# Performance work log

Hardware: AMD Instinct MI355X
Metric: run time of the kernel (lower is better)

## Reference

```python
import jax, jax.numpy as jnp
import numpy as np

N_EXPERTS = 8
TOP_K = 2


def setup_inputs() -> dict:
    key = jax.random.key(0)
    k1, k2, k3, k4 = jax.random.split(key, 4)
    B, T, C, H, E = 2, 2048, 1024, 4096, N_EXPERTS
    x = jax.random.normal(k1, (B, T, C), dtype=jnp.float32)
    # weights scaled like standard init to keep activations well-behaved
    router_w = jax.random.normal(k2, (E, C), dtype=jnp.float32) * 0.02
    w1 = jax.random.normal(k3, (E, C, H), dtype=jnp.float32) * (1.0 / np.sqrt(C))
    w2 = jax.random.normal(k4, (E, H, C), dtype=jnp.float32) * (1.0 / np.sqrt(H))
    return {"x": x, "router_w": router_w, "w1": w1, "w2": w2}


def reference(x, router_w, w1, w2):
    B, T, C = x.shape
    E = N_EXPERTS
    xf = x.reshape(-1, C)                                   # [N, C], N = B*T
    logits = jnp.einsum('nc,ec->ne', xf, router_w)          # router (no bias)
    probs = jax.nn.softmax(logits, axis=-1)
    top_w, top_i = jax.lax.top_k(probs, TOP_K)              # [N, K]
    top_w = top_w / jnp.sum(top_w, axis=-1, keepdims=True)  # renormalize
    # combine weight per (token, expert): sum of top-k weights routed to e
    comb = jnp.einsum('nk,nke->ne', top_w, jax.nn.one_hot(top_i, E, dtype=xf.dtype))
    # dense all-expert compute (bias=False, exact GELU, dropout=0 at eval)
    h = jax.nn.gelu(jnp.einsum('nc,ech->enh', xf, w1), approximate=False)  # [E, N, H]
    y = jnp.einsum('enh,ehc->enc', h, w2)                   # [E, N, C]
    out = jnp.einsum('ne,enc->nc', comb, y)                 # weighted combine
    return out.reshape(B, T, C)
```

## Files before the change

### kernel.cpp

```cpp
#include <hip/hip_runtime.h>
#include <hip/hip_bf16.h>
#include <stdint.h>

#define NTOK 4096
#define CD   1024
#define HD   4096
#define NE   8

typedef __attribute__((ext_vector_type(8))) short bf16x8;
typedef __attribute__((ext_vector_type(4))) float f32x4;
typedef __attribute__((ext_vector_type(4))) unsigned short us4;

__device__ __forceinline__ unsigned short f2bf(float f){
  __hip_bfloat16 h = __float2bfloat16(f);
  return *reinterpret_cast<unsigned short*>(&h);
}

__global__ __launch_bounds__(256) void router_kernel(
    const float* __restrict__ x, const float* __restrict__ rw,
    unsigned short* __restrict__ x_bf, int* __restrict__ top_i,
    float* __restrict__ top_w, int* __restrict__ counts){
  __shared__ float rw_lds[NE*CD];
  int tid = threadIdx.x;
  for (int i = tid; i < NE*CD/4; i += 256)
    ((float4*)rw_lds)[i] = ((const float4*)rw)[i];
  __syncthreads();
  int l = tid & 63, w = tid >> 6;
  int n = blockIdx.x*4 + w;

  float4 xv[4];
  #pragma unroll
  for (int j = 0; j < 4; ++j)
    xv[j] = ((const float4*)(x + (size_t)n*CD))[l + j*64];

  #pragma unroll
  for (int j = 0; j < 4; ++j){
    us4 o; o.x = f2bf(xv[j].x); o.y = f2bf(xv[j].y); o.z = f2bf(xv[j].z); o.w = f2bf(xv[j].w);
    *(us4*)(x_bf + (size_t)n*CD + l*4 + j*256) = o;
  }

  double le[NE];
  #pragma unroll
  for (int e = 0; e < NE; ++e){
    double p = 0.0;
    #pragma unroll
    for (int j = 0; j < 4; ++j){
      float4 rv = ((const float4*)(rw_lds + e*CD))[l + j*64];
      p += (double)xv[j].x*rv.x + (double)xv[j].y*rv.y + (double)xv[j].z*rv.z + (double)xv[j].w*rv.w;
    }
    #pragma unroll
    for (int d = 32; d >= 1; d >>= 1) p += __shfl_xor(p, d);
    le[e] = p;
  }
  if (l == 0){
    double m = le[0];
    #pragma unroll
    for (int e = 1; e < NE; ++e) m = le[e] > m ? le[e] : m;
    double pe[NE];
    #pragma unroll
    for (int e = 0; e < NE; ++e) pe[e] = exp(le[e]-m);
    int i0 = 0;
    #pragma unroll
    for (int e = 1; e < NE; ++e) if (pe[e] > pe[i0]) i0 = e;
    int i1 = (i0 == 0) ? 1 : 0;
    #pragma unroll
    for (int e = 0; e < NE; ++e){ if (e == i0) continue; if (pe[e] > pe[i1]) i1 = e; }
    double w0 = pe[i0], w1v = pe[i1], wsum = w0 + w1v;
    top_i[2*n] = i0; top_i[2*n+1] = i1;
    top_w[2*n] = (float)(w0/wsum); top_w[2*n+1] = (float)(w1v/wsum);
    atomicAdd(&counts[i0], 1); atomicAdd(&counts[i1], 1);
  }
}

__global__ void scan_kernel(const int* __restrict__ counts, int* __restrict__ offsets, int* __restrict__ cursor){
  if (threadIdx.x == 0){
    int s = 0;
    for (int e = 0; e < NE; ++e){ offsets[e] = s; cursor[e] = s; s += counts[e]; }
  }
}

__global__ __launch_bounds__(256) void scatter_kernel(
    const int* __restrict__ top_i, const float* __restrict__ top_w,
    int* __restrict__ cursor, int* __restrict__ g_tok, float* __restrict__ g_w){
  int n = blockIdx.x*256 + threadIdx.x;
  #pragma unroll
  for (int k = 0; k < 2; ++k){
    int e = top_i[2*n+k];
    int pos = atomicAdd(&cursor[e], 1);
    g_tok[pos] = n;
    g_w[pos] = top_w[2*n+k];
  }
}

template<int R, int S>
__global__ __launch_bounds__(256) void transpose_cvt(const float* __restrict__ in, unsigned short* __restrict__ outp){
  __shared__ float tile[64][65];
  int e = blockIdx.z;
  const float* ip = in + (size_t)e*R*S;
  unsigned short* op = outp + (size_t)e*R*S;
  int s0 = blockIdx.x*64, r0 = blockIdx.y*64;
  int tid = threadIdx.x;
  #pragma unroll
  for (int i = 0; i < 4; ++i){
    int lin = i*256 + tid;
    int rr = lin >> 4, c4 = lin & 15;
    float4 v = *(const float4*)(ip + (size_t)(r0+rr)*S + s0 + c4*4);
    tile[rr][c4*4+0] = v.x; tile[rr][c4*4+1] = v.y;
    tile[rr][c4*4+2] = v.z; tile[rr][c4*4+3] = v.w;
  }
  __syncthreads();
  #pragma unroll
  for (int i = 0; i < 4; ++i){
    int lin = i*256 + tid;
    int ss = lin >> 4, rq = lin & 15;
    us4 o;
    o.x = f2bf(tile[rq*4+0][ss]);
    o.y = f2bf(tile[rq*4+1][ss]);
    o.z = f2bf(tile[rq*4+2][ss]);
    o.w = f2bf(tile[rq*4+3][ss]);
    *(us4*)(op + (size_t)(s0+ss)*R + r0 + rq*4) = o;
  }
}

template<int KLEN, int SPLITK, int EPI>
__global__ __launch_bounds__(512, 6) void gemm2ph(
    const unsigned short* __restrict__ A_src,
    const unsigned short* __restrict__ B_src,
    unsigned short* __restrict__ h_out,
    float* __restrict__ outp,
    const int* __restrict__ g_tok,
    const float* __restrict__ g_w,
    const int* __restrict__ counts,
    const int* __restrict__ offsets,
    int NDIM, int KSTRIDE){
  constexpr int NT = KLEN/32;
  __shared__ alignas(128) char lds[32768];

  int z = blockIdx.z;
  int e  = (SPLITK == 1) ? z : (z / SPLITK);
  int kz = (SPLITK == 1) ? 0 : (z % SPLITK);
  int n_e = counts[e];
  int m0 = blockIdx.y*128;
  if (m0 >= n_e) return;
  int n0 = blockIdx.x*128;
  int g_base = offsets[e];
  int kstart = kz*KLEN;

  int tid = threadIdx.x, l = tid & 63, w = tid >> 6;
  int wr = w >> 2, wc = w & 3;
  int lrow = l & 15, q = l >> 4;

  const unsigned short* src[2];
  uint32_t dst[2];
  #pragma unroll
  for (int i = 0; i < 2; ++i){
    int g = i*512 + tid;
    bool isA = g < 512;
    int gg = isA ? g : (g - 512);
    int row = gg >> 2, c = gg & 3;
    int cs = c ^ (row & 3);
    if (isA){
      int rg = m0 + row; if (rg > n_e-1) rg = n_e-1;
      size_t arow;
      if (EPI == 0) arow = (size_t)g_tok[g_base + rg];
      else          arow = (size_t)(g_base + rg);
      src[i] = A_src + arow*(size_t)KSTRIDE + kstart + cs*8;
    } else {
      src[i] = B_src + ((size_t)e*NDIM + n0 + row)*(size_t)KSTRIDE + kstart + cs*8;
    }
    dst[i] = (uint32_t)g*16u;
  }

  uint32_t a_off[4], b_off[2];
  #pragma unroll
  for (int m = 0; m < 4; ++m){
    int ra = wr*64 + m*16 + lrow;
    a_off[m] = (uint32_t)(ra*64) + 16u*(q ^ (ra & 3));
  }
  #pragma unroll
  for (int n = 0; n < 2; ++n){
    int rb = wc*32 + n*16 + lrow;
    b_off[n] = 8192u + (uint32_t)(rb*64) + 16u*(q ^ (rb & 3));
  }

  f32x4 acc[4][2] = {};

  #pragma unroll
  for (int i = 0; i < 2; ++i){
    __builtin_amdgcn_global_load_lds((const __attribute__((address_space(1))) void*)src[i],
                                     (__attribute__((address_space(3))) void*)&lds[dst[i]], 16, 0, 0);
    src[i] += 32;
  }
  __syncthreads();

  uint32_t buf = 0;
  #pragma unroll 1
  for (int kt = 0; kt < NT; ++kt){
    if (kt + 1 < NT){
      uint32_t nb = (buf ^ 1)*16384u;
      #pragma unroll
      for (int i = 0; i < 2; ++i){
        __builtin_amdgcn_global_load_lds((const __attribute__((address_space(1))) void*)src[i],
                                         (__attribute__((address_space(3))) void*)&lds[dst[i] + nb], 16, 0, 0);
        src[i] += 32;
      }
    }
    uint32_t ro = buf*16384u;
    bf16x8 av[4], bv[2];
    #pragma unroll
    for (int m = 0; m < 4; ++m)
      av[m] = *(const bf16x8*)&lds[a_off[m] + ro];
    #pragma unroll
    for (int n = 0; n < 2; ++n)
      bv[n] = *(const bf16x8*)&lds[b_off[n] + ro];
    __builtin_amdgcn_s_setprio(1);
    #pragma unroll
    for (int m = 0; m < 4; ++m)
      #pragma unroll
      for (int n = 0; n < 2; ++n)
        acc[m][n] = __builtin_amdgcn_mfma_f32_16x16x32_bf16(av[m], bv[n], acc[m][n], 0, 0, 0);
    __builtin_amdgcn_s_setprio(0);
    __syncthreads();
    buf ^= 1;
  }

  if (EPI == 0){
    #pragma unroll
    for (int m = 0; m < 4; ++m){
      #pragma unroll
      for (int j = 0; j < 4; ++j){
        int r = m0 + wr*64 + m*16 + q*4 + j;
        if (r < n_e){
          unsigned short* hp = h_out + (size_t)(g_base + r)*NDIM + n0 + wc*32 + lrow;
          #pragma unroll
          for (int n = 0; n < 2; ++n){
            float v = acc[m][n][j];
            v = 0.5f*v*(1.0f + erff(v*0.70710678118654752f));
            hp[n*16] = f2bf(v);
          }
        }
      }
    }
  } else {
    #pragma unroll
    for (int m = 0; m < 4; ++m){
      #pragma unroll
      for (int j = 0; j < 4; ++j){
        int r = m0 + wr*64 + m*16 + q*4 + j;
        if (r < n_e){
          int slot = g_base + r;
          int t = g_tok[slot];
          float wgt = g_w[slot];
          float* op = outp + (size_t)t*NDIM + n0 + wc*32 + lrow;
          #pragma unroll
          for (int n = 0; n < 2; ++n)
            atomicAdd(op + n*16, wgt*acc[m][n][j]);
        }
      }
    }
  }
}

extern "C" void kernel_launch(void* const* d_in, const int* in_sizes, int n_in,
                              void* d_out, int out_size, void* d_ws, size_t ws_size,
                              hipStream_t stream) {
  const float* x  = (const float*)d_in[0];
  const float* rw = (const float*)d_in[1];
  const float* w1 = (const float*)d_in[2];
  const float* w2 = (const float*)d_in[3];

  size_t off = 0;
  auto alloc = [&](size_t sz) -> char* {
    char* p = (char*)d_ws + off;
    off += (sz + 255) & ~(size_t)255;
    return p;
  };
  unsigned short* x_bf = (unsigned short*)alloc((size_t)NTOK*CD*2);
  unsigned short* w1t  = (unsigned short*)alloc((size_t)NE*CD*HD*2);
  unsigned short* w2t  = (unsigned short*)alloc((size_t)NE*CD*HD*2);
  unsigned short* hbuf = (unsigned short*)alloc((size_t)NTOK*2*HD*2);
  int*   top_i  = (int*)alloc(NTOK*2*4);
  float* top_w  = (float*)alloc(NTOK*2*4);
  int*   counts = (int*)alloc(64);
  int*   offs   = (int*)alloc(64);
  int*   cursor = (int*)alloc(64);
  int*   g_tok  = (int*)alloc(NTOK*2*4);
  float* g_w    = (float*)alloc(NTOK*2*4);
  (void)ws_size; (void)in_sizes; (void)n_in; (void)out_size;

  hipMemsetAsync(d_out, 0, (size_t)NTOK*CD*4, stream);
  hipMemsetAsync(counts, 0, 64, stream);

  router_kernel<<<dim3(NTOK/4), dim3(256), 0, stream>>>(x, rw, x_bf, top_i, top_w, counts);
  scan_kernel<<<dim3(1), dim3(64), 0, stream>>>(counts, offs, cursor);
  scatter_kernel<<<dim3(NTOK/256), dim3(256), 0, stream>>>(top_i, top_w, cursor, g_tok, g_w);

  transpose_cvt<CD, HD><<<dim3(HD/64, CD/64, NE), dim3(256), 0, stream>>>(w1, w1t);
  transpose_cvt<HD, CD><<<dim3(CD/64, HD/64, NE), dim3(256), 0, stream>>>(w2, w2t);

  gemm2ph<CD, 1, 0><<<dim3(HD/128, 12, NE), dim3(512), 0, stream>>>(
      x_bf, w1t, hbuf, (float*)nullptr, g_tok, g_w, counts, offs, HD, CD);
  gemm2ph<HD/2, 2, 1><<<dim3(CD/128, 12, NE*2), dim3(512), 0, stream>>>(
      hbuf, w2t, (unsigned short*)nullptr, (float*)d_out, g_tok, g_w, counts, offs, CD, HD);
}
```

Before: 477.9 us.

## Use three-stage LDS ring with explicit vmcnt waits in grouped GEMMs

Replaces the double-buffered LDS pipeline with a three-slot ring buffer that prefetches two k-tiles ahead. It waits with explicit s_waitcnt vmcnt counts and issues a single raw s_barrier per iteration, where the old loop had a full __syncthreads at the end. The goal is to keep more global-to-LDS loads in flight and cut barrier stalls. In exchange LDS per block grows from 32KB to 48KB, which may lower occupancy. The hand-written waitcnt values assume the compiler emits exactly two loads per stage.

```diff
diff --git a/kernel.cpp b/kernel.cpp
--- a/kernel.cpp
+++ b/kernel.cpp
@@ -10,6 +10,10 @@
 typedef __attribute__((ext_vector_type(8))) short bf16x8;
 typedef __attribute__((ext_vector_type(4))) float f32x4;
 typedef __attribute__((ext_vector_type(4))) unsigned short us4;
+
+#define BARR() asm volatile("s_barrier" ::: "memory")
+#define VM2() asm volatile("s_waitcnt vmcnt(2)" ::: "memory")
+#define VM0() asm volatile("s_waitcnt vmcnt(0)" ::: "memory")
 
 __device__ __forceinline__ unsigned short f2bf(float f){
   __hip_bfloat16 h = __float2bfloat16(f);
@@ -123,7 +127,7 @@
 }
 
 template<int KLEN, int SPLITK, int EPI>
-__global__ __launch_bounds__(512, 6) void gemm2ph(
+__global__ __launch_bounds__(512, 6) void gemm_ring3(
     const unsigned short* __restrict__ A_src,
     const unsigned short* __restrict__ B_src,
     unsigned short* __restrict__ h_out,
@@ -134,7 +138,7 @@
     const int* __restrict__ offsets,
     int NDIM, int KSTRIDE){
   constexpr int NT = KLEN/32;
-  __shared__ alignas(128) char lds[32768];
+  __shared__ alignas(128) char lds[49152];
 
   int z = blockIdx.z;
   int e  = (SPLITK == 1) ? z : (z / SPLITK);
@@ -171,6 +175,14 @@
     dst[i] = (uint32_t)g*16u;
   }
 
+  auto STAGE = [&](int t, uint32_t bufoff){
+    #pragma unroll
+    for (int i = 0; i < 2; ++i)
+      __builtin_amdgcn_global_load_lds(
+        (const __attribute__((address_space(1))) void*)(src[i] + (size_t)t*32),
+        (__attribute__((address_space(3))) void*)&lds[dst[i] + bufoff], 16, 0, 0);
+  };
+
   uint32_t a_off[4], b_off[2];
   #pragma unroll
   for (int m = 0; m < 4; ++m){
@@ -185,27 +197,15 @@
 
   f32x4 acc[4][2] = {};
 
-  #pragma unroll
-  for (int i = 0; i < 2; ++i){
-    __builtin_amdgcn_global_load_lds((const __attribute__((address_space(1))) void*)src[i],
-                                     (__attribute__((address_space(3))) void*)&lds[dst[i]], 16, 0, 0);
-    src[i] += 32;
-  }
-  __syncthreads();
-
-  uint32_t buf = 0;
+  STAGE(0, 0u); STAGE(1, 16384u);
+
+  uint32_t ro = 0u;
+  uint32_t so = 32768u;
   #pragma unroll 1
   for (int kt = 0; kt < NT; ++kt){
-    if (kt + 1 < NT){
-      uint32_t nb = (buf ^ 1)*16384u;
-      #pragma unroll
-      for (int i = 0; i < 2; ++i){
-        __builtin_amdgcn_global_load_lds((const __attribute__((address_space(1))) void*)src[i],
-                                         (__attribute__((address_space(3))) void*)&lds[dst[i] + nb], 16, 0, 0);
-        src[i] += 32;
-      }
-    }
-    uint32_t ro = buf*16384u;
+    if (kt < NT-1) { VM2(); } else { VM0(); }
+    BARR();
+    if (kt + 2 < NT) STAGE(kt + 2, so);
     bf16x8 av[4], bv[2];
     #pragma unroll
     for (int m = 0; m < 4; ++m)
@@ -220,8 +220,8 @@
       for (int n = 0; n < 2; ++n)
         acc[m][n] = __builtin_amdgcn_mfma_f32_16x16x32_bf16(av[m], bv[n], acc[m][n], 0, 0, 0);
     __builtin_amdgcn_s_setprio(0);
-    __syncthreads();
-    buf ^= 1;
+    ro = (ro == 32768u) ? 0u : ro + 16384u;
+    so = (so == 32768u) ? 0u : so + 16384u;
   }
 
   if (EPI == 0){
@@ -298,8 +298,8 @@
   transpose_cvt<CD, HD><<<dim3(HD/64, CD/64, NE), dim3(256), 0, stream>>>(w1, w1t);
   transpose_cvt<HD, CD><<<dim3(CD/64, HD/64, NE), dim3(256), 0, stream>>>(w2, w2t);
 
-  gemm2ph<CD, 1, 0><<<dim3(HD/128, 12, NE), dim3(512), 0, stream>>>(
+  gemm_ring3<CD, 1, 0><<<dim3(HD/128, 12, NE), dim3(512), 0, stream>>>(
       x_bf, w1t, hbuf, (float*)nullptr, g_tok, g_w, counts, offs, HD, CD);
-  gemm2ph<HD/2, 2, 1><<<dim3(CD/128, 12, NE*2), dim3(512), 0, stream>>>(
+  gemm_ring3<HD/2, 2, 1><<<dim3(CD/128, 12, NE*2), dim3(512), 0, stream>>>(
       hbuf, w2t, (unsigned short*)nullptr, (float*)d_out, g_tok, g_w, counts, offs, CD, HD);
 }
```

Result: faster. 457.9 us (-4.2%).
